# Kernel optimization log

Measured on AMD Instinct MI355X. Metric: run time of the kernel, lower is better.

The kernel has to match this reference:

```python
import jax, jax.numpy as jnp
import numpy as np

B, L, NUM_AA, E, H = 128, 2048, 20, 16, 128

def _mlp(x, W1, b1, W2, b2, W3, b3):
    h = jax.nn.relu(x @ W1 + b1)
    h = jax.nn.relu(h @ W2 + b2)
    return h @ W3 + b3

def _mlp_params(key, in_dim):
    k1, k2, k3 = jax.random.split(key, 3)
    W1 = jax.random.normal(k1, (in_dim, H), jnp.float32) / np.sqrt(in_dim)
    W2 = jax.random.normal(k2, (H, H), jnp.float32) / np.sqrt(H)
    W3 = jax.random.normal(k3, (H, 1), jnp.float32) / np.sqrt(H)
    return W1, jnp.zeros((H,), jnp.float32), W2, jnp.zeros((H,), jnp.float32), W3, jnp.zeros((1,), jnp.float32)

def setup_inputs() -> dict:
    key = jax.random.key(0)
    kR, ks, ke, kl, kt, kp = jax.random.split(key, 6)
    inp = {
        'R': jax.random.normal(kR, (B, L, 3), jnp.float32) * 3.8,  # ~CA-CA scale
        'seq': jax.random.randint(ks, (B, L), 0, NUM_AA),
        'emb': jax.random.normal(ke, (NUM_AA, E), jnp.float32),
    }
    for pref, k, d in (('fl', kl, 1 + 2 * E), ('ft', kt, 1 + 3 * E), ('fp', kp, 2 + 4 * E)):
        W1, b1, W2, b2, W3, b3 = _mlp_params(k, d)
        inp.update({f'{pref}_W1': W1, f'{pref}_b1': b1, f'{pref}_W2': W2, f'{pref}_b2': b2, f'{pref}_W3': W3, f'{pref}_b3': b3})
    return inp

def _energy(R, e, fl, ft, fp):
    d = R[:, 1:, :] - R[:, :-1, :]                      # [B,L-1,3] bond vectors
    lengths = jnp.linalg.norm(d, axis=-1)               # [B,L-1]
    x_l = jnp.concatenate([lengths[..., None], e[:, :-1, :], e[:, 1:, :]], axis=-1)
    E_l = _mlp(x_l, *fl)[..., 0].sum(axis=1)
    # bond angles at atom i+1 between (R[i]-R[i+1]) and (R[i+2]-R[i+1])
    u, v = -d[:, :-1, :], d[:, 1:, :]                   # [B,L-2,3]
    cos_t = jnp.sum(u * v, axis=-1) / (jnp.linalg.norm(u, axis=-1) * jnp.linalg.norm(v, axis=-1))
    theta_in = jnp.clip(cos_t, -1.0, 1.0)               # use_cos_theta=True -> cos(arccos(clip))
    x_t = jnp.concatenate([theta_in[..., None], e[:, :-2, :], e[:, 1:-1, :], e[:, 2:, :]], axis=-1)
    E_t = _mlp(x_t, *ft)[..., 0].sum(axis=1)
    # torsions over quadruples
    b1, b2, b3 = d[:, :-2, :], d[:, 1:-1, :], d[:, 2:, :]
    n1 = jnp.cross(b1, b2)
    n2 = jnp.cross(b2, b3)
    b2u = b2 / jnp.linalg.norm(b2, axis=-1, keepdims=True)
    m1 = jnp.cross(n1, b2u)
    phi = jnp.arctan2(jnp.sum(m1 * n2, axis=-1), jnp.sum(n1 * n2, axis=-1))  # [B,L-3]
    sc = jnp.stack([jnp.sin(phi), jnp.cos(phi)], axis=-1)                    # [B,L-3,2]
    x_p = jnp.concatenate([sc, e[:, :-3, :], e[:, 1:-2, :], e[:, 2:-1, :], e[:, 3:, :]], axis=-1)
    E_p = _mlp(x_p, *fp)[..., 0].sum(axis=1)
    return E_l + E_t + E_p

def reference(R, seq, emb,
              fl_W1, fl_b1, fl_W2, fl_b2, fl_W3, fl_b3,
              ft_W1, ft_b1, ft_W2, ft_b2, ft_W3, ft_b3,
              fp_W1, fp_b1, fp_W2, fp_b2, fp_W3, fp_b3):
    e = emb[seq]                                        # [B,L,E]
    return _energy(R, e,
                   (fl_W1, fl_b1, fl_W2, fl_b2, fl_W3, fl_b3),
                   (ft_W1, ft_b1, ft_W2, ft_b2, ft_W3, ft_b3),
                   (fp_W1, fp_b1, fp_W2, fp_b2, fp_W3, fp_b3))
```

## Files before the change

kernel.cpp:

```cpp
#include <hip/hip_runtime.h>


typedef short bf16x8  __attribute__((ext_vector_type(8)));
typedef float f32x4   __attribute__((ext_vector_type(4)));
typedef float f32x16  __attribute__((ext_vector_type(16)));

constexpr int Lc  = 2048;
constexpr int SHs = 136;

union FragU { uint4 u; bf16x8 v; };

__device__ __forceinline__ unsigned short f2bf(float f) {
    union { float f; unsigned u; } v; v.f = f;
    unsigned u = v.u;
    u = u + 0x7FFFu + ((u >> 16) & 1u);
    return (unsigned short)(u >> 16);
}

__device__ __forceinline__ unsigned pkbf(float a, float b) {
    unsigned ua = __float_as_uint(a) + 0x8000u;
    unsigned ub = __float_as_uint(b) + 0x8000u;
    return __builtin_amdgcn_perm(ub, ua, 0x07060302u);
}

__global__ __launch_bounds__(256)
void prep_kernel(const float* __restrict__ W1_0, const float* __restrict__ b1_0,
                 const float* __restrict__ W1_1, const float* __restrict__ b1_1,
                 const float* __restrict__ W1_2, const float* __restrict__ b1_2,
                 const float* __restrict__ W2_0, const float* __restrict__ W2_1,
                 const float* __restrict__ W2_2,
                 const float* __restrict__ emb, char* __restrict__ ws,
                 float* __restrict__ out)
{
    const int tid = blockIdx.x * 256 + threadIdx.x;
    const int np  = gridDim.x * 256;
    if (blockIdx.x == 0 && threadIdx.x < 128) out[threadIdx.x] = 0.0f;

    unsigned short* d2 = (unsigned short*)ws;
    for (int o = tid; o < 3 * 16384; o += np) {
        int t = o >> 14, r = o & 16383, col = r >> 7, k = r & 127;
        const float* W2 = (t == 0) ? W2_0 : (t == 1) ? W2_1 : W2_2;
        d2[o] = f2bf(W2[k * 128 + col]);
    }
    unsigned short* d1 = (unsigned short*)(ws + 98304);
    for (int o = tid; o < 3 * 12288; o += np) {
        int t = o / 12288, r = o - t * 12288, hid = r / 96, k = r - hid * 96;
        const int NE16 = (t == 0) ? 32 : (t == 1) ? 48 : 64;
        const int NG   = (t == 2) ? 2 : 1;
        const float* W1 = (t == 0) ? W1_0 : (t == 1) ? W1_1 : W1_2;
        const float* b1 = (t == 0) ? b1_0 : (t == 1) ? b1_1 : b1_2;
        float v = 0.0f;
        if (k >= 16) {
            int j = k - 16;
            if (j < NE16) v = W1[(NG + j) * 128 + hid];
        } else if (k == 4) v = b1[hid];
        else if (t == 0 && k == 0) v = W1_0[hid];
        else if (t == 1 && k == 1) v = W1_1[hid];
        else if (t == 2 && k == 2) v = W1_2[hid];
        else if (t == 2 && k == 3) v = W1_2[128 + hid];
        d1[o] = f2bf(v);
    }
    unsigned short* eb = (unsigned short*)(ws + 172032);
    for (int i = tid; i < 320; i += np) eb[i] = f2bf(emb[i]);
}

struct SMem {
    unsigned short H1s[128 * SHs];
    float  Rbuf[393];
    uint2  geomh[128];
    int    seqb[132];
    unsigned short ebuf[320];
    float  part[4];
};

template<int TYPE>
__device__ __forceinline__ void type_pass(
    SMem& sm, const char* __restrict__ ws,
    const float* __restrict__ b2, const float* __restrict__ w3,
    int i0, int wv, int ln31, int hi, f32x4& p4)
{
    constexpr int NEMB  = (TYPE == 0) ? 2 : (TYPE == 1) ? 3 : 4;
    constexpr int STEPS = 1 + NEMB;
    constexpr int ROWSB = Lc - 1 - TYPE;

    const unsigned short* w1t = (const unsigned short*)(ws + 98304 + TYPE * 24576);
    const unsigned short* w2t = (const unsigned short*)(ws + TYPE * 32768);
    const f32x4 z4 = (f32x4){0.f, 0.f, 0.f, 0.f};

    FragU A1[STEPS];
#pragma unroll
    for (int s = 0; s < STEPS; ++s)
        A1[s].u = *(const uint4*)&w1t[(wv * 32 + ln31) * 96 + s * 16 + hi * 8];

#pragma unroll
    for (int h = 0; h < 2; ++h) {
        f32x16 acc1[2];
        acc1[0] = (f32x16)(0.f);
        acc1[1] = (f32x16)(0.f);

#pragma unroll
        for (int s = 0; s < STEPS; ++s) {
#pragma unroll
            for (int rt = 0; rt < 2; ++rt) {
                const int row = h * 64 + rt * 32 + ln31;
                FragU bb;
                if (s == 0) {
                    if (hi == 0) {
                        uint2 g = sm.geomh[row];
                        bb.u = make_uint4(g.x, g.y, 0x00003F80u, 0u);
                    } else {
                        bb.u = make_uint4(0u, 0u, 0u, 0u);
                    }
                } else {
                    bb.u = *(const uint4*)&sm.ebuf[sm.seqb[row + (s - 1)] * 16 + hi * 8];
                }
                acc1[rt] = __builtin_amdgcn_mfma_f32_32x32x16_bf16(A1[s].v, bb.v, acc1[rt], 0, 0, 0);
            }
        }

#pragma unroll
        for (int rt = 0; rt < 2; ++rt) {
            const int row = h * 64 + rt * 32 + ln31;
#pragma unroll
            for (int g = 0; g < 4; ++g) {
                float v0 = fmaxf(acc1[rt][4 * g + 0], 0.f);
                float v1 = fmaxf(acc1[rt][4 * g + 1], 0.f);
                float v2 = fmaxf(acc1[rt][4 * g + 2], 0.f);
                float v3 = fmaxf(acc1[rt][4 * g + 3], 0.f);
                uint2 pk;
                pk.x = pkbf(v0, v1);
                pk.y = pkbf(v2, v3);
                *(uint2*)&sm.H1s[row * SHs + wv * 32 + 8 * g + 4 * hi] = pk;
            }
        }
    }

    FragU B2[8];
#pragma unroll
    for (int s2 = 0; s2 < 8; ++s2)
        B2[s2].u = *(const uint4*)&w2t[(wv * 32 + ln31) * 128 + s2 * 16 + hi * 8];
    const float b2v = b2[wv * 32 + ln31];
    const float w3v = w3[wv * 32 + ln31];
    __syncthreads();

#pragma unroll
    for (int h = 0; h < 2; ++h) {
        f32x16 acc2[2];
        acc2[0] = (f32x16)(0.f);
        acc2[1] = (f32x16)(0.f);
#pragma unroll
        for (int s2 = 0; s2 < 8; ++s2)
#pragma unroll
            for (int rt = 0; rt < 2; ++rt) {
                const int row = h * 64 + rt * 32 + ln31;
                bf16x8 aa = *(const bf16x8*)&sm.H1s[row * SHs + s2 * 16 + hi * 8];
                acc2[rt] = __builtin_amdgcn_mfma_f32_32x32x16_bf16(aa, B2[s2].v, acc2[rt], 0, 0, 0);
            }

#pragma unroll
        for (int rt = 0; rt < 2; ++rt) {
#pragma unroll
            for (int g = 0; g < 4; ++g) {
                const int rbase = i0 + h * 64 + rt * 32 + 8 * g + 4 * hi;
                f32x4 v;
                v[0] = acc2[rt][4 * g + 0]; v[1] = acc2[rt][4 * g + 1];
                v[2] = acc2[rt][4 * g + 2]; v[3] = acc2[rt][4 * g + 3];
                v = __builtin_elementwise_max(v + b2v, z4);
                if (rbase + 3 < ROWSB) {
                    p4 += v * w3v;
                } else {
#pragma unroll
                    for (int rg = 0; rg < 4; ++rg)
                        if (rbase + rg < ROWSB) p4[rg] += v[rg] * w3v;
                }
            }
        }
    }
    __syncthreads();
}

__global__ __launch_bounds__(256, 4)
void energy_kernel(const float* __restrict__ R, const int* __restrict__ seq,
                   const char* __restrict__ ws,
                   const float* b2_0, const float* b2_1, const float* b2_2,
                   const float* w3_0, const float* w3_1, const float* w3_2,
                   const float* b3_0, const float* b3_1, const float* b3_2,
                   float* __restrict__ out)
{
    __shared__ SMem sm;
    const int tid = threadIdx.x;
    const int b   = blockIdx.y;
    const int i0  = blockIdx.x * 128;
    const int lane = tid & 63, wv = tid >> 6;
    const int ln31 = lane & 31, hi = lane >> 5;

    for (int t = tid; t < 393; t += 256) {
        int lr = t / 3, comp = t - lr * 3;
        int row = min(i0 + lr, Lc - 1);
        sm.Rbuf[t] = R[((size_t)b * Lc + row) * 3 + comp];
    }
    for (int t = tid; t < 131; t += 256)
        sm.seqb[t] = seq[b * Lc + min(i0 + t, Lc - 1)];
    {
        const uint4* se = (const uint4*)(ws + 172032);
        for (int t = tid; t < 40; t += 256) ((uint4*)sm.ebuf)[t] = se[t];
    }
    __syncthreads();

    if (tid < 128) {
        const float* p0 = &sm.Rbuf[tid * 3];
        float ax = p0[3] - p0[0], ay = p0[4] - p0[1], az = p0[5] - p0[2];
        float bx = p0[6] - p0[3], by = p0[7] - p0[4], bz = p0[8] - p0[5];
        float cx = p0[9] - p0[6], cy = p0[10] - p0[7], cz = p0[11] - p0[8];
        float na2 = ax * ax + ay * ay + az * az;
        float len = sqrtf(na2);
        float nb2 = bx * bx + by * by + bz * bz;
        float duv = -(ax * bx + ay * by + az * bz);
        float cost = fminf(fmaxf(duv / sqrtf(na2 * nb2), -1.0f), 1.0f);
        float n1x = ay * bz - az * by, n1y = az * bx - ax * bz, n1z = ax * by - ay * bx;
        float n2x = by * cz - bz * cy, n2y = bz * cx - bx * cz, n2z = bx * cy - by * cx;
        float binv = 1.0f / sqrtf(nb2);
        float ux = bx * binv, uy = by * binv, uz = bz * binv;
        float m1x = n1y * uz - n1z * uy, m1y = n1z * ux - n1x * uz, m1z = n1x * uy - n1y * ux;
        float yv = m1x * n2x + m1y * n2y + m1z * n2z;
        float xv = n1x * n2x + n1y * n2y + n1z * n2z;
        float inv = 1.0f / sqrtf(xv * xv + yv * yv);
        sm.geomh[tid] = make_uint2(pkbf(len, cost), pkbf(yv * inv, xv * inv));
    }
    __syncthreads();

    f32x4 p4 = (f32x4){0.f, 0.f, 0.f, 0.f};
    type_pass<0>(sm, ws, b2_0, w3_0, i0, wv, ln31, hi, p4);
    type_pass<1>(sm, ws, b2_1, w3_1, i0, wv, ln31, hi, p4);
    type_pass<2>(sm, ws, b2_2, w3_2, i0, wv, ln31, hi, p4);

    float p = p4[0] + p4[1] + p4[2] + p4[3];
#pragma unroll
    for (int off = 32; off > 0; off >>= 1)
        p += __shfl_down(p, off);
    if (lane == 0) sm.part[wv] = p;
    __syncthreads();
    if (tid == 0) {
        float tot = sm.part[0] + sm.part[1] + sm.part[2] + sm.part[3];
        tot += b3_0[0] * (float)min(Lc - 1 - i0, 128);
        tot += b3_1[0] * (float)min(Lc - 2 - i0, 128);
        tot += b3_2[0] * (float)min(Lc - 3 - i0, 128);
        atomicAdd(&out[b], tot);
    }
}

extern "C" void kernel_launch(void* const* d_in, const int* in_sizes, int n_in,
                              void* d_out, int out_size, void* d_ws, size_t ws_size,
                              hipStream_t stream) {
    const float* R   = (const float*)d_in[0];
    const int*   seq = (const int*)d_in[1];
    const float* emb = (const float*)d_in[2];
    float* out = (float*)d_out;
    char*  ws  = (char*)d_ws;

    prep_kernel<<<dim3(96), dim3(256), 0, stream>>>(
        (const float*)d_in[3],  (const float*)d_in[4],
        (const float*)d_in[9],  (const float*)d_in[10],
        (const float*)d_in[15], (const float*)d_in[16],
        (const float*)d_in[5],  (const float*)d_in[11], (const float*)d_in[17],
        emb, ws, out);

    dim3 grid(16, 128), block(256);
    energy_kernel<<<grid, block, 0, stream>>>(
        R, seq, ws,
        (const float*)d_in[6],  (const float*)d_in[12], (const float*)d_in[18],
        (const float*)d_in[7],  (const float*)d_in[13], (const float*)d_in[19],
        (const float*)d_in[8],  (const float*)d_in[14], (const float*)d_in[20],
        out);
}
```

Baseline: 154.4 us.

## Software-pipeline layer-1 and layer-2 MFMA stages with double-buffered hidden tile

Splits each MLP type pass into a layer-1 stage that writes a 64-row half-tile of hidden activations and a layer-2 stage that consumes it, using two LDS buffers. Layer-1 of the next half-tile is interleaved with layer-2 of the previous one, so there is one barrier per stage instead of two per type and more independent MFMA work between barriers. Launch bounds drop from 4 to 3 blocks per CU to leave room for the extra live registers, which may reduce occupancy.

Measured after the change: 159.3 us. 3.2% more time.

```diff
diff --git a/kernel.cpp b/kernel.cpp
--- a/kernel.cpp
+++ b/kernel.cpp
@@ -65,7 +65,7 @@
 }
 
 struct SMem {
-    unsigned short H1s[128 * SHs];
+    unsigned short H1d[2][64 * SHs];
     float  Rbuf[393];
     uint2  geomh[128];
     int    seqb[132];
@@ -73,67 +73,68 @@
     float  part[4];
 };
 
-template<int TYPE>
-__device__ __forceinline__ void type_pass(
-    SMem& sm, const char* __restrict__ ws,
-    const float* __restrict__ b2, const float* __restrict__ w3,
-    int i0, int wv, int ln31, int hi, f32x4& p4)
+template<int TYPE, int H, int BUF>
+__device__ __forceinline__ void g1_stage(SMem& sm, const char* __restrict__ ws,
+                                         int wv, int ln31, int hi)
 {
     constexpr int NEMB  = (TYPE == 0) ? 2 : (TYPE == 1) ? 3 : 4;
     constexpr int STEPS = 1 + NEMB;
+    const unsigned short* w1t = (const unsigned short*)(ws + 98304 + TYPE * 24576);
+
+    FragU A1[STEPS];
+#pragma unroll
+    for (int s = 0; s < STEPS; ++s)
+        A1[s].u = *(const uint4*)&w1t[(wv * 32 + ln31) * 96 + s * 16 + hi * 8];
+
+    f32x16 acc1[2];
+    acc1[0] = (f32x16)(0.f);
+    acc1[1] = (f32x16)(0.f);
+
+#pragma unroll
+    for (int s = 0; s < STEPS; ++s)
+#pragma unroll
+        for (int rt = 0; rt < 2; ++rt) {
+            const int row = H * 64 + rt * 32 + ln31;
+            FragU bb;
+            if (s == 0) {
+                if (hi == 0) {
+                    uint2 g = sm.geomh[row];
+                    bb.u = make_uint4(g.x, g.y, 0x00003F80u, 0u);
+                } else {
+                    bb.u = make_uint4(0u, 0u, 0u, 0u);
+                }
+            } else {
+                bb.u = *(const uint4*)&sm.ebuf[sm.seqb[row + (s - 1)] * 16 + hi * 8];
+            }
+            acc1[rt] = __builtin_amdgcn_mfma_f32_32x32x16_bf16(A1[s].v, bb.v, acc1[rt], 0, 0, 0);
+        }
+
+#pragma unroll
+    for (int rt = 0; rt < 2; ++rt) {
+        const int rl = rt * 32 + ln31;
+#pragma unroll
+        for (int g = 0; g < 4; ++g) {
+            float v0 = fmaxf(acc1[rt][4 * g + 0], 0.f);
+            float v1 = fmaxf(acc1[rt][4 * g + 1], 0.f);
+            float v2 = fmaxf(acc1[rt][4 * g + 2], 0.f);
+            float v3 = fmaxf(acc1[rt][4 * g + 3], 0.f);
+            uint2 pk;
+            pk.x = pkbf(v0, v1);
+            pk.y = pkbf(v2, v3);
+            *(uint2*)&sm.H1d[BUF][rl * SHs + wv * 32 + 8 * g + 4 * hi] = pk;
+        }
+    }
+}
+
+template<int TYPE, int H, int BUF>
+__device__ __forceinline__ void g2_stage(SMem& sm, const char* __restrict__ ws,
+                                         const float* __restrict__ b2,
+                                         const float* __restrict__ w3,
+                                         int i0, int wv, int ln31, int hi, f32x4& p4)
+{
     constexpr int ROWSB = Lc - 1 - TYPE;
-
-    const unsigned short* w1t = (const unsigned short*)(ws + 98304 + TYPE * 24576);
     const unsigned short* w2t = (const unsigned short*)(ws + TYPE * 32768);
     const f32x4 z4 = (f32x4){0.f, 0.f, 0.f, 0.f};
-
-    FragU A1[STEPS];
-#pragma unroll
-    for (int s = 0; s < STEPS; ++s)
-        A1[s].u = *(const uint4*)&w1t[(wv * 32 + ln31) * 96 + s * 16 + hi * 8];
-
-#pragma unroll
-    for (int h = 0; h < 2; ++h) {
-        f32x16 acc1[2];
-        acc1[0] = (f32x16)(0.f);
-        acc1[1] = (f32x16)(0.f);
-
-#pragma unroll
-        for (int s = 0; s < STEPS; ++s) {
-#pragma unroll
-            for (int rt = 0; rt < 2; ++rt) {
-                const int row = h * 64 + rt * 32 + ln31;
-                FragU bb;
-                if (s == 0) {
-                    if (hi == 0) {
-                        uint2 g = sm.geomh[row];
-                        bb.u = make_uint4(g.x, g.y, 0x00003F80u, 0u);
-                    } else {
-                        bb.u = make_uint4(0u, 0u, 0u, 0u);
-                    }
-                } else {
-                    bb.u = *(const uint4*)&sm.ebuf[sm.seqb[row + (s - 1)] * 16 + hi * 8];
-                }
-                acc1[rt] = __builtin_amdgcn_mfma_f32_32x32x16_bf16(A1[s].v, bb.v, acc1[rt], 0, 0, 0);
-            }
-        }
-
-#pragma unroll
-        for (int rt = 0; rt < 2; ++rt) {
-            const int row = h * 64 + rt * 32 + ln31;
-#pragma unroll
-            for (int g = 0; g < 4; ++g) {
-                float v0 = fmaxf(acc1[rt][4 * g + 0], 0.f);
-                float v1 = fmaxf(acc1[rt][4 * g + 1], 0.f);
-                float v2 = fmaxf(acc1[rt][4 * g + 2], 0.f);
-                float v3 = fmaxf(acc1[rt][4 * g + 3], 0.f);
-                uint2 pk;
-                pk.x = pkbf(v0, v1);
-                pk.y = pkbf(v2, v3);
-                *(uint2*)&sm.H1s[row * SHs + wv * 32 + 8 * g + 4 * hi] = pk;
-            }
-        }
-    }
 
     FragU B2[8];
 #pragma unroll
@@ -141,45 +142,38 @@
         B2[s2].u = *(const uint4*)&w2t[(wv * 32 + ln31) * 128 + s2 * 16 + hi * 8];
     const float b2v = b2[wv * 32 + ln31];
     const float w3v = w3[wv * 32 + ln31];
-    __syncthreads();
-
-#pragma unroll
-    for (int h = 0; h < 2; ++h) {
-        f32x16 acc2[2];
-        acc2[0] = (f32x16)(0.f);
-        acc2[1] = (f32x16)(0.f);
-#pragma unroll
-        for (int s2 = 0; s2 < 8; ++s2)
-#pragma unroll
-            for (int rt = 0; rt < 2; ++rt) {
-                const int row = h * 64 + rt * 32 + ln31;
-                bf16x8 aa = *(const bf16x8*)&sm.H1s[row * SHs + s2 * 16 + hi * 8];
-                acc2[rt] = __builtin_amdgcn_mfma_f32_32x32x16_bf16(aa, B2[s2].v, acc2[rt], 0, 0, 0);
+
+    f32x16 acc2[2];
+    acc2[0] = (f32x16)(0.f);
+    acc2[1] = (f32x16)(0.f);
+#pragma unroll
+    for (int s2 = 0; s2 < 8; ++s2)
+#pragma unroll
+        for (int rt = 0; rt < 2; ++rt) {
+            bf16x8 aa = *(const bf16x8*)&sm.H1d[BUF][(rt * 32 + ln31) * SHs + s2 * 16 + hi * 8];
+            acc2[rt] = __builtin_amdgcn_mfma_f32_32x32x16_bf16(aa, B2[s2].v, acc2[rt], 0, 0, 0);
+        }
+
+#pragma unroll
+    for (int rt = 0; rt < 2; ++rt)
+#pragma unroll
+        for (int g = 0; g < 4; ++g) {
+            const int rbase = i0 + H * 64 + rt * 32 + 8 * g + 4 * hi;
+            f32x4 v;
+            v[0] = acc2[rt][4 * g + 0]; v[1] = acc2[rt][4 * g + 1];
+            v[2] = acc2[rt][4 * g + 2]; v[3] = acc2[rt][4 * g + 3];
+            v = __builtin_elementwise_max(v + b2v, z4);
+            if (rbase + 3 < ROWSB) {
+                p4 += v * w3v;
+            } else {
+#pragma unroll
+                for (int rg = 0; rg < 4; ++rg)
+                    if (rbase + rg < ROWSB) p4[rg] += v[rg] * w3v;
             }
-
-#pragma unroll
-        for (int rt = 0; rt < 2; ++rt) {
-#pragma unroll
-            for (int g = 0; g < 4; ++g) {
-                const int rbase = i0 + h * 64 + rt * 32 + 8 * g + 4 * hi;
-                f32x4 v;
-                v[0] = acc2[rt][4 * g + 0]; v[1] = acc2[rt][4 * g + 1];
-                v[2] = acc2[rt][4 * g + 2]; v[3] = acc2[rt][4 * g + 3];
-                v = __builtin_elementwise_max(v + b2v, z4);
-                if (rbase + 3 < ROWSB) {
-                    p4 += v * w3v;
-                } else {
-#pragma unroll
-                    for (int rg = 0; rg < 4; ++rg)
-                        if (rbase + rg < ROWSB) p4[rg] += v[rg] * w3v;
-                }
-            }
-        }
-    }
-    __syncthreads();
-}
-
-__global__ __launch_bounds__(256, 4)
+        }
+}
+
+__global__ __launch_bounds__(256, 3)
 void energy_kernel(const float* __restrict__ R, const int* __restrict__ seq,
                    const char* __restrict__ ws,
                    const float* b2_0, const float* b2_1, const float* b2_2,
@@ -230,9 +224,25 @@
     __syncthreads();
 
     f32x4 p4 = (f32x4){0.f, 0.f, 0.f, 0.f};
-    type_pass<0>(sm, ws, b2_0, w3_0, i0, wv, ln31, hi, p4);
-    type_pass<1>(sm, ws, b2_1, w3_1, i0, wv, ln31, hi, p4);
-    type_pass<2>(sm, ws, b2_2, w3_2, i0, wv, ln31, hi, p4);
+
+    g1_stage<0, 0, 0>(sm, ws, wv, ln31, hi);
+    __syncthreads();
+    g1_stage<0, 1, 1>(sm, ws, wv, ln31, hi);
+    g2_stage<0, 0, 0>(sm, ws, b2_0, w3_0, i0, wv, ln31, hi, p4);
+    __syncthreads();
+    g1_stage<1, 0, 0>(sm, ws, wv, ln31, hi);
+    g2_stage<0, 1, 1>(sm, ws, b2_0, w3_0, i0, wv, ln31, hi, p4);
+    __syncthreads();
+    g1_stage<1, 1, 1>(sm, ws, wv, ln31, hi);
+    g2_stage<1, 0, 0>(sm, ws, b2_1, w3_1, i0, wv, ln31, hi, p4);
+    __syncthreads();
+    g1_stage<2, 0, 0>(sm, ws, wv, ln31, hi);
+    g2_stage<1, 1, 1>(sm, ws, b2_1, w3_1, i0, wv, ln31, hi, p4);
+    __syncthreads();
+    g1_stage<2, 1, 1>(sm, ws, wv, ln31, hi);
+    g2_stage<2, 0, 0>(sm, ws, b2_2, w3_2, i0, wv, ln31, hi, p4);
+    __syncthreads();
+    g2_stage<2, 1, 1>(sm, ws, b2_2, w3_2, i0, wv, ln31, hi, p4);
 
     float p = p4[0] + p4[1] + p4[2] + p4[3];
 #pragma unroll
```
